# Optimization experiments

Hardware: AMD Instinct MI355X
Metric: run time of the kernel (lower is better)

Reference implementation:

```python
import jax, jax.numpy as jnp
import numpy as np

HEADS = 8
DIM_HEAD = 32
SCALE = DIM_HEAD ** (-0.5)


def setup_inputs() -> dict:
    key = jax.random.key(0)
    k1, k2, k3, k4 = jax.random.split(key, 4)
    x = jax.random.normal(k1, (16, 256, 64, 64), dtype=jnp.float32)
    # conv 1x1 weights stored as [out_ch, in_ch]
    w_qkv = jax.random.normal(k2, (3 * HEADS * DIM_HEAD, 256), dtype=jnp.float32) * 0.05
    w_out = jax.random.normal(k3, (256, HEADS * DIM_HEAD), dtype=jnp.float32) * 0.05
    b_out = jax.random.normal(k4, (256,), dtype=jnp.float32) * 0.05
    return {"x": x, "w_qkv": w_qkv, "w_out": w_out, "b_out": b_out}


def reference(x, w_qkv, w_out, b_out):
    b, c, h, w = x.shape
    n = h * w
    # 1x1 conv (no bias) == channel matmul
    qkv = jnp.einsum('bchw,oc->bohw', x, w_qkv)            # [b, 3*H*D, h, w]
    qkv = qkv.reshape(b, 3, HEADS, DIM_HEAD, n)            # chunk then 'b (h c) xy'
    q, k, v = qkv[:, 0], qkv[:, 1], qkv[:, 2]              # [b, H, D, n]
    q = jax.nn.softmax(q, axis=-2) * SCALE                 # softmax over channel dim d
    k = jax.nn.softmax(k, axis=-1)                         # softmax over spatial n
    context = jnp.einsum('bhdn,bhen->bhde', k, v)          # [b, H, D, D]
    out = jnp.einsum('bhde,bhdn->bhen', context, q)        # [b, H, D, n]
    out = out.reshape(b, HEADS * DIM_HEAD, h, w)
    # 1x1 conv with bias
    return jnp.einsum('bchw,oc->bohw', out, w_out) + b_out[None, :, None, None]
```

## Files before the change

kernel.cpp:

```cpp
#include <hip/hip_runtime.h>
#include <cstddef>
#include <cstdint>

#define NN 4096
#define CIN 256
#define CQKV 768
#define NBATCH 16
#define QSCALE 0.17677669529663687f

typedef short s16x8 __attribute__((ext_vector_type(8)));
typedef float f32x4 __attribute__((ext_vector_type(4)));

__device__ __forceinline__ float bf2f(unsigned short u) {
    unsigned int x = ((unsigned int)u) << 16;
    return __builtin_bit_cast(float, x);
}
__device__ __forceinline__ unsigned short f2bf(float f) {
    unsigned int u = __builtin_bit_cast(unsigned int, f);
    return (unsigned short)((u + 0x7fffu + ((u >> 16) & 1u)) >> 16);
}
__device__ __forceinline__ void glds16(const void* gsrc, void* lds) {
    __builtin_amdgcn_global_load_lds(
        (const __attribute__((address_space(1))) unsigned int*)gsrc,
        (__attribute__((address_space(3))) unsigned int*)lds,
        16, 0, 0);
}

__global__ __launch_bounds__(256)
void xpose(const float* __restrict__ x, unsigned short* __restrict__ xT)
{
    const int b = blockIdx.z;
    const int n0 = blockIdx.x * 64, c0 = blockIdx.y * 64;
    __shared__ float xs[64][65];
    const int t = threadIdx.x;
    const float* xb = x + (size_t)b * CIN * NN;
#pragma unroll
    for (int p = 0; p < 4; ++p) {
        const int row = p * 16 + (t >> 4);
        const int col = (t & 15) * 4;
        const float4 v = *reinterpret_cast<const float4*>(
            &xb[(size_t)(c0 + row) * NN + n0 + col]);
        xs[col + 0][row] = v.x; xs[col + 1][row] = v.y;
        xs[col + 2][row] = v.z; xs[col + 3][row] = v.w;
    }
    __syncthreads();
    const int n = t >> 2, cch = (t & 3) * 16;
    unsigned short arr[16];
#pragma unroll
    for (int e = 0; e < 16; ++e) arr[e] = f2bf(xs[n][cch + e]);
    unsigned short* dst = xT + ((size_t)b * NN + n0 + n) * 256 + c0 + cch;
    *reinterpret_cast<s16x8*>(&dst[0]) = *reinterpret_cast<s16x8*>(&arr[0]);
    *reinterpret_cast<s16x8*>(&dst[8]) = *reinterpret_cast<s16x8*>(&arr[8]);
}

__global__ __launch_bounds__(256)
void wcvt(const float* __restrict__ w, unsigned short* __restrict__ wb)
{
    const int i = (blockIdx.x * 256 + threadIdx.x) * 4;
    const float4 v = *reinterpret_cast<const float4*>(&w[i]);
    unsigned short a[4] = { f2bf(v.x), f2bf(v.y), f2bf(v.z), f2bf(v.w) };
    *reinterpret_cast<ushort2*>(&wb[i])     = *reinterpret_cast<ushort2*>(&a[0]);
    *reinterpret_cast<ushort2*>(&wb[i + 2]) = *reinterpret_cast<ushort2*>(&a[2]);
}

__device__ __forceinline__ void gemm_pipe(const unsigned short* __restrict__ Ab,
                                          const unsigned short* __restrict__ Bb,
                                          int m0, int n0, char* smem,
                                          f32x4 (&acc)[4][4])
{
    const int t = threadIdx.x;
    const int lane = t & 63, w = t >> 6;
    const int lr = lane & 15, lq = lane >> 4;
    const int wr = (w >> 1) * 64, wc = (w & 1) * 64;
    const int ch0 = (w * 2 + 0) * 64 + lane;
    const int ch1 = (w * 2 + 1) * 64 + lane;
    const int r0 = ch0 >> 2, c0s = (ch0 & 3) ^ ((r0 >> 1) & 3);
    const int r1 = ch1 >> 2, c1s = (ch1 & 3) ^ ((r1 >> 1) & 3);
    char* Abuf = smem;
    char* Bbuf = smem + 32768;

#define STG_H(h)                                                               \
  { char* ab = Abuf + ((h) & 3) * 8192;                                        \
    char* bb = Bbuf + ((h) & 3) * 8192;                                        \
    glds16(Ab + (size_t)(m0 + r0) * 256 + (h) * 32 + c0s * 8, ab + (w*2+0)*1024); \
    glds16(Ab + (size_t)(m0 + r1) * 256 + (h) * 32 + c1s * 8, ab + (w*2+1)*1024); \
    glds16(Bb + (size_t)(n0 + r0) * 256 + (h) * 32 + c0s * 8, bb + (w*2+0)*1024); \
    glds16(Bb + (size_t)(n0 + r1) * 256 + (h) * 32 + c1s * 8, bb + (w*2+1)*1024); }

#define CMP_H(h)                                                               \
  { char* ab = Abuf + ((h) & 3) * 8192;                                        \
    char* bb = Bbuf + ((h) & 3) * 8192;                                        \
    s16x8 af[4], bfr[4];                                                       \
    _Pragma("unroll") for (int m = 0; m < 4; ++m) {                            \
        const int row = wr + m * 16 + lr;                                      \
        af[m] = *(const s16x8*)(ab + row * 64 + ((lq ^ ((row >> 1) & 3)) << 4)); } \
    _Pragma("unroll") for (int n = 0; n < 4; ++n) {                            \
        const int col = wc + n * 16 + lr;                                      \
        bfr[n] = *(const s16x8*)(bb + col * 64 + ((lq ^ ((col >> 1) & 3)) << 4)); } \
    __builtin_amdgcn_s_setprio(1);                                             \
    _Pragma("unroll") for (int m = 0; m < 4; ++m)                              \
    _Pragma("unroll") for (int n = 0; n < 4; ++n)                              \
        acc[m][n] = __builtin_amdgcn_mfma_f32_16x16x32_bf16(af[m], bfr[n],     \
                                                            acc[m][n], 0, 0, 0); \
    __builtin_amdgcn_s_setprio(0); }

    STG_H(0); STG_H(1); STG_H(2);
#pragma unroll
    for (int i = 0; i < 8; ++i) {
        if (i < 6)       asm volatile("s_waitcnt vmcnt(8)" ::: "memory");
        else if (i == 6) asm volatile("s_waitcnt vmcnt(4)" ::: "memory");
        else             asm volatile("s_waitcnt vmcnt(0)" ::: "memory");
        __builtin_amdgcn_s_barrier();
        __builtin_amdgcn_sched_barrier(0);
        if (i < 5) STG_H(i + 3);
        CMP_H(i);
    }
#undef STG_H
#undef CMP_H
}

__global__ __launch_bounds__(256, 2)
void qkv_fused(const unsigned short* __restrict__ wb,
               const unsigned short* __restrict__ xT,
               unsigned short* __restrict__ qT,
               float* __restrict__ ctx_part,
               float* __restrict__ z_part)
{
    __shared__ __align__(16) char smem[65536];
    const int nt = blockIdx.x;
    const int ty = blockIdx.y;
    const int b  = blockIdx.z;
    const int t = threadIdx.x;
    const int lane = t & 63, w = t >> 6;
    const int lr = lane & 15, lq = lane >> 4;
    const int wr = (w >> 1) * 64, wc = (w & 1) * 64;
    const int n0 = nt * 128;

    if (ty < 2) {
        const int m0 = ty * 128;
        const unsigned short* Bb = xT + (size_t)b * NN * 256;
        f32x4 acc[4][4] = {};
        gemm_pipe(wb, Bb, m0, n0, smem, acc);

        __syncthreads();
        unsigned short (*qs)[136] = (unsigned short (*)[136])smem;
#pragma unroll
        for (int n = 0; n < 4; ++n) {
            const int col = wc + n * 16 + lr;
#pragma unroll
            for (int hp = 0; hp < 2; ++hp) {
                float mx = -1e30f;
#pragma unroll
                for (int u = 0; u < 2; ++u)
#pragma unroll
                    for (int r = 0; r < 4; ++r)
                        mx = fmaxf(mx, acc[hp * 2 + u][n][r]);
                mx = fmaxf(mx, __shfl_xor(mx, 16));
                mx = fmaxf(mx, __shfl_xor(mx, 32));
                float er[2][4];
                float s = 0.f;
#pragma unroll
                for (int u = 0; u < 2; ++u)
#pragma unroll
                    for (int r = 0; r < 4; ++r) {
                        er[u][r] = __expf(acc[hp * 2 + u][n][r] - mx);
                        s += er[u][r];
                    }
                s += __shfl_xor(s, 16);
                s += __shfl_xor(s, 32);
                const float inv = QSCALE / s;
#pragma unroll
                for (int u = 0; u < 2; ++u) {
                    ushort4 pk;
                    pk.x = f2bf(er[u][0] * inv);
                    pk.y = f2bf(er[u][1] * inv);
                    pk.z = f2bf(er[u][2] * inv);
                    pk.w = f2bf(er[u][3] * inv);
                    *(ushort4*)&qs[col][wr + (hp * 2 + u) * 16 + lq * 4] = pk;
                }
            }
        }
        __syncthreads();
        const int nl = t >> 1, half = t & 1;
        const unsigned short* src = &qs[nl][half * 64];
        unsigned short* dst = qT + ((size_t)b * NN + n0 + nl) * 256 + m0 + half * 64;
#pragma unroll
        for (int i = 0; i < 8; ++i)
            *(s16x8*)(dst + i * 8) = *(const s16x8*)(src + i * 8);
    } else {
        const int g = ty - 2;
        const unsigned short* An = xT + ((size_t)b * NN + (size_t)n0) * 256;

        f32x4 acc[4][4] = {};
        gemm_pipe(An, wb, 0, 256 + g * 128, smem, acc);

        unsigned int ekpk[4][4][2];
        float zl[4] = {0.f, 0.f, 0.f, 0.f};
#pragma unroll
        for (int m = 0; m < 4; ++m)
#pragma unroll
            for (int nn = 0; nn < 4; ++nn) {
                const unsigned short u0 = f2bf(__expf(acc[m][nn][0]));
                const unsigned short u1 = f2bf(__expf(acc[m][nn][1]));
                const unsigned short u2 = f2bf(__expf(acc[m][nn][2]));
                const unsigned short u3 = f2bf(__expf(acc[m][nn][3]));
                zl[nn] += bf2f(u0) + bf2f(u1) + bf2f(u2) + bf2f(u3);
                ekpk[m][nn][0] = (unsigned int)u0 | ((unsigned int)u1 << 16);
                ekpk[m][nn][1] = (unsigned int)u2 | ((unsigned int)u3 << 16);
            }
#pragma unroll
        for (int nn = 0; nn < 4; ++nn) {
            zl[nn] += __shfl_xor(zl[nn], 16);
            zl[nn] += __shfl_xor(zl[nn], 32);
        }
        const float zv = (lq == 0) ? zl[0] : (lq == 1) ? zl[1] : (lq == 2) ? zl[2] : zl[3];
        z_part[((((size_t)(b * 32 + nt)) * 2 + g) * 2 + (w >> 1)) * 128 + wc + lane] = zv;

#pragma unroll
        for (int m = 0; m < 4; ++m)
#pragma unroll
            for (int nn = 0; nn < 4; ++nn) acc[m][nn] = (f32x4){0.f, 0.f, 0.f, 0.f};
        gemm_pipe(An, wb, 0, 512 + g * 128, smem, acc);

        __syncthreads();
#pragma unroll
        for (int m = 0; m < 4; ++m)
#pragma unroll
            for (int nn = 0; nn < 4; ++nn) {
                const int col = wc + nn * 16 + lr;
                const int swz = (col & 7) << 4;
                const int rowb = (wr + m * 16 + lq * 4) * 2;
                *(unsigned int*)(smem + ((col * 256 + rowb) ^ swz))       = ekpk[m][nn][0];
                *(unsigned int*)(smem + ((col * 256 + rowb + 4) ^ swz))   = ekpk[m][nn][1];
                const unsigned int vp0 = (unsigned int)f2bf(acc[m][nn][0])
                                       | ((unsigned int)f2bf(acc[m][nn][1]) << 16);
                const unsigned int vp1 = (unsigned int)f2bf(acc[m][nn][2])
                                       | ((unsigned int)f2bf(acc[m][nn][3]) << 16);
                *(unsigned int*)(smem + 32768 + ((col * 256 + rowb) ^ swz))     = vp0;
                *(unsigned int*)(smem + 32768 + ((col * 256 + rowb + 4) ^ swz)) = vp1;
            }
        __syncthreads();

        f32x4 cacc[2][2] = {};
#pragma unroll
        for (int ks = 0; ks < 4; ++ks) {
            s16x8 af[2], bfv[2];
#pragma unroll
            for (int dt = 0; dt < 2; ++dt) {
                const int drow = w * 32 + dt * 16 + lr;
                af[dt] = *(const s16x8*)(smem +
                    ((drow * 256 + ks * 64 + lq * 16) ^ ((drow & 7) << 4)));
            }
#pragma unroll
            for (int et = 0; et < 2; ++et) {
                const int erow = w * 32 + et * 16 + lr;
                bfv[et] = *(const s16x8*)(smem + 32768 +
                    ((erow * 256 + ks * 64 + lq * 16) ^ ((erow & 7) << 4)));
            }
#pragma unroll
            for (int dt = 0; dt < 2; ++dt)
#pragma unroll
                for (int et = 0; et < 2; ++et)
                    cacc[dt][et] = __builtin_amdgcn_mfma_f32_16x16x32_bf16(
                        af[dt], bfv[et], cacc[dt][et], 0, 0, 0);
        }
        float* cp = ctx_part + ((((size_t)(b * 32 + nt)) * 2 + g) * 4 + w) * 1024;
#pragma unroll
        for (int dt = 0; dt < 2; ++dt)
#pragma unroll
            for (int et = 0; et < 2; ++et)
#pragma unroll
                for (int r = 0; r < 4; ++r)
                    cp[(dt * 16 + lq * 4 + r) * 32 + et * 16 + lr] = cacc[dt][et][r];
    }
}

__global__ __launch_bounds__(256)
void make_m(const float* __restrict__ ctx_part, const float* __restrict__ z_part,
            const float* __restrict__ w_out, unsigned short* __restrict__ Mmat)
{
    const int h = blockIdx.x, b = blockIdx.y;
    const int g = h >> 2, hh = h & 3;
    const int t = threadIdx.x;
    __shared__ float ctx[32][33];
    __shared__ float zinv[32];

    for (int c = t; c < 1024; c += 256) {
        float s = 0.f;
#pragma unroll 8
        for (int nt = 0; nt < 32; ++nt)
            s += ctx_part[((((size_t)(b * 32 + nt)) * 2 + g) * 4 + hh) * 1024 + c];
        ctx[c >> 5][c & 31] = s;
    }
    if (t < 32) {
        float z = 0.f;
#pragma unroll 8
        for (int nt = 0; nt < 32; ++nt) {
            const size_t base = (((size_t)(b * 32 + nt)) * 2 + g) * 2;
            z += z_part[(base + 0) * 128 + hh * 32 + t];
            z += z_part[(base + 1) * 128 + hh * 32 + t];
        }
        zinv[t] = 1.f / z;
    }
    __syncthreads();

    const int o = t;
    float wrow[32];
#pragma unroll
    for (int e = 0; e < 32; ++e)
        wrow[e] = w_out[(size_t)o * 256 + h * 32 + e];
#pragma unroll 4
    for (int d = 0; d < 32; ++d) {
        float s = 0.f;
#pragma unroll
        for (int e = 0; e < 32; ++e)
            s = fmaf(wrow[e], ctx[d][e], s);
        Mmat[((size_t)b * 256 + o) * 256 + h * 32 + d] = f2bf(s * zinv[d]);
    }
}

__global__ __launch_bounds__(256, 2)
void gemm_out(const unsigned short* __restrict__ Mmat,
              const unsigned short* __restrict__ qT,
              float* __restrict__ out, const float* __restrict__ bias)
{
    __shared__ __align__(16) char smem[65536];
    const int bz = blockIdx.z;
    const int m0 = blockIdx.y * 128, n0 = blockIdx.x * 128;
    const unsigned short* Ab = Mmat + (size_t)bz * 256 * 256;
    const unsigned short* Bb = qT + (size_t)bz * NN * 256;

    f32x4 acc[4][4] = {};
    gemm_pipe(Ab, Bb, m0, n0, smem, acc);

    const int t = threadIdx.x;
    const int lane = t & 63, w = t >> 6;
    const int lr = lane & 15, lq = lane >> 4;
    const int wr = (w >> 1) * 64, wc = (w & 1) * 64;

    __syncthreads();
#pragma unroll
    for (int m = 0; m < 4; ++m)
#pragma unroll
        for (int r = 0; r < 4; ++r) {
            const int row = wr + m * 16 + lq * 4 + r;
            const float bv = bias[m0 + row];
            const int rb = row * 512;
            const int xs = (row & 7) << 4;
#pragma unroll
            for (int n = 0; n < 4; ++n) {
                const int col = wc + n * 16 + lr;
                *(float*)(smem + rb + ((col * 4) ^ xs)) = acc[m][n][r] + bv;
            }
        }
    __syncthreads();

    float* Yb = out + (size_t)bz * CIN * NN;
#pragma unroll
    for (int p = 0; p < 8; ++p) {
        const int row = p * 16 + (t >> 4);
        const int rb = row * 512;
        const int xs = (row & 7) << 4;
        const int cb = (t & 15) * 32;
        const float4 v0 = *(const float4*)(smem + rb + ((cb + 0) ^ xs));
        const float4 v1 = *(const float4*)(smem + rb + ((cb + 16) ^ xs));
        float* dst = Yb + (size_t)(m0 + row) * NN + n0 + (t & 15) * 8;
        *(float4*)dst = v0;
        *(float4*)(dst + 4) = v1;
    }
}

extern "C" void kernel_launch(void* const* d_in, const int* in_sizes, int n_in,
                              void* d_out, int out_size, void* d_ws, size_t ws_size,
                              hipStream_t stream)
{
    const float* x     = (const float*)d_in[0];
    const float* w_qkv = (const float*)d_in[1];
    const float* w_out = (const float*)d_in[2];
    const float* b_out = (const float*)d_in[3];
    float* out = (float*)d_out;

    char* ws = (char*)d_ws;
    size_t off = 0;
    unsigned short* xT  = (unsigned short*)(ws + off);  off += (size_t)NBATCH * NN * CIN * 2;
    unsigned short* qT  = (unsigned short*)(ws + off);  off += (size_t)NBATCH * NN * CIN * 2;
    float* ctx_part     = (float*)(ws + off);           off += (size_t)NBATCH * 32 * 2 * 4 * 1024 * 4;
    float* z_part       = (float*)(ws + off);           off += (size_t)NBATCH * 32 * 2 * 2 * 128 * 4;
    unsigned short* Mmat= (unsigned short*)(ws + off);  off += (size_t)NBATCH * 256 * 256 * 2;
    unsigned short* wb  = (unsigned short*)(ws + off);  off += (size_t)CQKV * CIN * 2;

    xpose<<<dim3(NN / 64, CIN / 64, NBATCH), 256, 0, stream>>>(x, xT);
    wcvt<<<dim3(CQKV * CIN / 1024), 256, 0, stream>>>(w_qkv, wb);

    qkv_fused<<<dim3(32, 4, NBATCH), 256, 0, stream>>>(wb, xT, qT, ctx_part, z_part);

    make_m<<<dim3(8, NBATCH), 256, 0, stream>>>(ctx_part, z_part, w_out, Mmat);

    gemm_out<<<dim3(32, 2, NBATCH), 256, 0, stream>>>(Mmat, qT, out, b_out);
}
```

Before: 107.3 us.

## Shrink GEMM pipeline to three LDS stages to fit three blocks per CU

The shared GEMM pipeline drops from a 4-deep to a 3-deep LDS ring buffer, cutting shared memory from 64KB to 48KB per block. Launch bounds rise to 3 blocks per CU. The epilogues of qkv_fused (context MFMA staging) and gemm_out (output transpose) are split into two half passes so they fit in the smaller LDS. More resident blocks should hide latency better, at the cost of less prefetch depth, extra barriers in the epilogues, and register pressure under the tighter launch bound.

```diff
diff --git a/kernel.cpp b/kernel.cpp
--- a/kernel.cpp
+++ b/kernel.cpp
@@ -63,10 +63,10 @@
     *reinterpret_cast<ushort2*>(&wb[i + 2]) = *reinterpret_cast<ushort2*>(&a[2]);
 }
 
-__device__ __forceinline__ void gemm_pipe(const unsigned short* __restrict__ Ab,
-                                          const unsigned short* __restrict__ Bb,
-                                          int m0, int n0, char* smem,
-                                          f32x4 (&acc)[4][4])
+__device__ __forceinline__ void gemm_pipe3(const unsigned short* __restrict__ Ab,
+                                           const unsigned short* __restrict__ Bb,
+                                           int m0, int n0, char* smem,
+                                           f32x4 (&acc)[4][4])
 {
     const int t = threadIdx.x;
     const int lane = t & 63, w = t >> 6;
@@ -77,19 +77,19 @@
     const int r0 = ch0 >> 2, c0s = (ch0 & 3) ^ ((r0 >> 1) & 3);
     const int r1 = ch1 >> 2, c1s = (ch1 & 3) ^ ((r1 >> 1) & 3);
     char* Abuf = smem;
-    char* Bbuf = smem + 32768;
+    char* Bbuf = smem + 24576;
 
 #define STG_H(h)                                                               \
-  { char* ab = Abuf + ((h) & 3) * 8192;                                        \
-    char* bb = Bbuf + ((h) & 3) * 8192;                                        \
+  { char* ab = Abuf + ((h) % 3) * 8192;                                        \
+    char* bb = Bbuf + ((h) % 3) * 8192;                                        \
     glds16(Ab + (size_t)(m0 + r0) * 256 + (h) * 32 + c0s * 8, ab + (w*2+0)*1024); \
     glds16(Ab + (size_t)(m0 + r1) * 256 + (h) * 32 + c1s * 8, ab + (w*2+1)*1024); \
     glds16(Bb + (size_t)(n0 + r0) * 256 + (h) * 32 + c0s * 8, bb + (w*2+0)*1024); \
     glds16(Bb + (size_t)(n0 + r1) * 256 + (h) * 32 + c1s * 8, bb + (w*2+1)*1024); }
 
 #define CMP_H(h)                                                               \
-  { char* ab = Abuf + ((h) & 3) * 8192;                                        \
-    char* bb = Bbuf + ((h) & 3) * 8192;                                        \
+  { char* ab = Abuf + ((h) % 3) * 8192;                                        \
+    char* bb = Bbuf + ((h) % 3) * 8192;                                        \
     s16x8 af[4], bfr[4];                                                       \
     _Pragma("unroll") for (int m = 0; m < 4; ++m) {                            \
         const int row = wr + m * 16 + lr;                                      \
@@ -104,29 +104,28 @@
                                                             acc[m][n], 0, 0, 0); \
     __builtin_amdgcn_s_setprio(0); }
 
-    STG_H(0); STG_H(1); STG_H(2);
+    STG_H(0); STG_H(1);
 #pragma unroll
     for (int i = 0; i < 8; ++i) {
-        if (i < 6)       asm volatile("s_waitcnt vmcnt(8)" ::: "memory");
-        else if (i == 6) asm volatile("s_waitcnt vmcnt(4)" ::: "memory");
-        else             asm volatile("s_waitcnt vmcnt(0)" ::: "memory");
+        if (i < 7) asm volatile("s_waitcnt vmcnt(4)" ::: "memory");
+        else       asm volatile("s_waitcnt vmcnt(0)" ::: "memory");
         __builtin_amdgcn_s_barrier();
         __builtin_amdgcn_sched_barrier(0);
-        if (i < 5) STG_H(i + 3);
+        if (i < 6) STG_H(i + 2);
         CMP_H(i);
     }
 #undef STG_H
 #undef CMP_H
 }
 
-__global__ __launch_bounds__(256, 2)
+__global__ __launch_bounds__(256, 3)
 void qkv_fused(const unsigned short* __restrict__ wb,
                const unsigned short* __restrict__ xT,
                unsigned short* __restrict__ qT,
                float* __restrict__ ctx_part,
                float* __restrict__ z_part)
 {
-    __shared__ __align__(16) char smem[65536];
+    __shared__ __align__(16) char smem[49152];
     const int nt = blockIdx.x;
     const int ty = blockIdx.y;
     const int b  = blockIdx.z;
@@ -140,7 +139,7 @@
         const int m0 = ty * 128;
         const unsigned short* Bb = xT + (size_t)b * NN * 256;
         f32x4 acc[4][4] = {};
-        gemm_pipe(wb, Bb, m0, n0, smem, acc);
+        gemm_pipe3(wb, Bb, m0, n0, smem, acc);
 
         __syncthreads();
         unsigned short (*qs)[136] = (unsigned short (*)[136])smem;
@@ -192,7 +191,7 @@
         const unsigned short* An = xT + ((size_t)b * NN + (size_t)n0) * 256;
 
         f32x4 acc[4][4] = {};
-        gemm_pipe(An, wb, 0, 256 + g * 128, smem, acc);
+        gemm_pipe3(An, wb, 0, 256 + g * 128, smem, acc);
 
         unsigned int ekpk[4][4][2];
         float zl[4] = {0.f, 0.f, 0.f, 0.f};
@@ -220,49 +219,58 @@
         for (int m = 0; m < 4; ++m)
 #pragma unroll
             for (int nn = 0; nn < 4; ++nn) acc[m][nn] = (f32x4){0.f, 0.f, 0.f, 0.f};
-        gemm_pipe(An, wb, 0, 512 + g * 128, smem, acc);
+        gemm_pipe3(An, wb, 0, 512 + g * 128, smem, acc);
 
         __syncthreads();
-#pragma unroll
-        for (int m = 0; m < 4; ++m)
-#pragma unroll
-            for (int nn = 0; nn < 4; ++nn) {
-                const int col = wc + nn * 16 + lr;
-                const int swz = (col & 7) << 4;
-                const int rowb = (wr + m * 16 + lq * 4) * 2;
-                *(unsigned int*)(smem + ((col * 256 + rowb) ^ swz))       = ekpk[m][nn][0];
-                *(unsigned int*)(smem + ((col * 256 + rowb + 4) ^ swz))   = ekpk[m][nn][1];
-                const unsigned int vp0 = (unsigned int)f2bf(acc[m][nn][0])
-                                       | ((unsigned int)f2bf(acc[m][nn][1]) << 16);
-                const unsigned int vp1 = (unsigned int)f2bf(acc[m][nn][2])
-                                       | ((unsigned int)f2bf(acc[m][nn][3]) << 16);
-                *(unsigned int*)(smem + 32768 + ((col * 256 + rowb) ^ swz))     = vp0;
-                *(unsigned int*)(smem + 32768 + ((col * 256 + rowb + 4) ^ swz)) = vp1;
+        f32x4 cacc[2][2] = {};
+#pragma unroll
+        for (int p = 0; p < 2; ++p) {
+            if ((w >> 1) == p) {
+#pragma unroll
+                for (int m = 0; m < 4; ++m)
+#pragma unroll
+                    for (int nn = 0; nn < 4; ++nn) {
+                        const int col = wc + nn * 16 + lr;
+                        const int swz = (col & 7) << 4;
+                        const int rowb = (m * 16 + lq * 4) * 2;
+                        *(unsigned int*)(smem + ((col * 128 + rowb) ^ swz))
+                            = ekpk[m][nn][0];
+                        *(unsigned int*)(smem + ((col * 128 + rowb + 4) ^ swz))
+                            = ekpk[m][nn][1];
+                        const unsigned int vp0 = (unsigned int)f2bf(acc[m][nn][0])
+                            | ((unsigned int)f2bf(acc[m][nn][1]) << 16);
+                        const unsigned int vp1 = (unsigned int)f2bf(acc[m][nn][2])
+                            | ((unsigned int)f2bf(acc[m][nn][3]) << 16);
+                        *(unsigned int*)(smem + 16384 +
+                            ((col * 128 + rowb) ^ swz)) = vp0;
+                        *(unsigned int*)(smem + 16384 +
+                            ((col * 128 + rowb + 4) ^ swz)) = vp1;
+                    }
             }
-        __syncthreads();
-
-        f32x4 cacc[2][2] = {};
-#pragma unroll
-        for (int ks = 0; ks < 4; ++ks) {
-            s16x8 af[2], bfv[2];
-#pragma unroll
-            for (int dt = 0; dt < 2; ++dt) {
-                const int drow = w * 32 + dt * 16 + lr;
-                af[dt] = *(const s16x8*)(smem +
-                    ((drow * 256 + ks * 64 + lq * 16) ^ ((drow & 7) << 4)));
+            __syncthreads();
+#pragma unroll
+            for (int ks2 = 0; ks2 < 2; ++ks2) {
+                s16x8 afk[2], bfv[2];
+#pragma unroll
+                for (int dt = 0; dt < 2; ++dt) {
+                    const int drow = w * 32 + dt * 16 + lr;
+                    afk[dt] = *(const s16x8*)(smem + drow * 128 +
+                        ((((ks2 * 4 + lq) ^ (drow & 7))) << 4));
+                }
+#pragma unroll
+                for (int et = 0; et < 2; ++et) {
+                    const int erow = w * 32 + et * 16 + lr;
+                    bfv[et] = *(const s16x8*)(smem + 16384 + erow * 128 +
+                        ((((ks2 * 4 + lq) ^ (erow & 7))) << 4));
+                }
+#pragma unroll
+                for (int dt = 0; dt < 2; ++dt)
+#pragma unroll
+                    for (int et = 0; et < 2; ++et)
+                        cacc[dt][et] = __builtin_amdgcn_mfma_f32_16x16x32_bf16(
+                            afk[dt], bfv[et], cacc[dt][et], 0, 0, 0);
             }
-#pragma unroll
-            for (int et = 0; et < 2; ++et) {
-                const int erow = w * 32 + et * 16 + lr;
-                bfv[et] = *(const s16x8*)(smem + 32768 +
-                    ((erow * 256 + ks * 64 + lq * 16) ^ ((erow & 7) << 4)));
-            }
-#pragma unroll
-            for (int dt = 0; dt < 2; ++dt)
-#pragma unroll
-                for (int et = 0; et < 2; ++et)
-                    cacc[dt][et] = __builtin_amdgcn_mfma_f32_16x16x32_bf16(
-                        af[dt], bfv[et], cacc[dt][et], 0, 0, 0);
+            __syncthreads();
         }
         float* cp = ctx_part + ((((size_t)(b * 32 + nt)) * 2 + g) * 4 + w) * 1024;
 #pragma unroll
@@ -319,54 +327,59 @@
     }
 }
 
-__global__ __launch_bounds__(256, 2)
+__global__ __launch_bounds__(256, 3)
 void gemm_out(const unsigned short* __restrict__ Mmat,
               const unsigned short* __restrict__ qT,
               float* __restrict__ out, const float* __restrict__ bias)
 {
-    __shared__ __align__(16) char smem[65536];
+    __shared__ __align__(16) char smem[49152];
     const int bz = blockIdx.z;
     const int m0 = blockIdx.y * 128, n0 = blockIdx.x * 128;
     const unsigned short* Ab = Mmat + (size_t)bz * 256 * 256;
     const unsigned short* Bb = qT + (size_t)bz * NN * 256;
 
     f32x4 acc[4][4] = {};
-    gemm_pipe(Ab, Bb, m0, n0, smem, acc);
+    gemm_pipe3(Ab, Bb, m0, n0, smem, acc);
 
     const int t = threadIdx.x;
     const int lane = t & 63, w = t >> 6;
     const int lr = lane & 15, lq = lane >> 4;
-    const int wr = (w >> 1) * 64, wc = (w & 1) * 64;
+    const int wc = (w & 1) * 64;
 
     __syncthreads();
-#pragma unroll
-    for (int m = 0; m < 4; ++m)
-#pragma unroll
-        for (int r = 0; r < 4; ++r) {
-            const int row = wr + m * 16 + lq * 4 + r;
-            const float bv = bias[m0 + row];
-            const int rb = row * 512;
-            const int xs = (row & 7) << 4;
-#pragma unroll
-            for (int n = 0; n < 4; ++n) {
-                const int col = wc + n * 16 + lr;
-                *(float*)(smem + rb + ((col * 4) ^ xs)) = acc[m][n][r] + bv;
-            }
-        }
-    __syncthreads();
-
     float* Yb = out + (size_t)bz * CIN * NN;
 #pragma unroll
-    for (int p = 0; p < 8; ++p) {
-        const int row = p * 16 + (t >> 4);
-        const int rb = row * 512;
-        const int xs = (row & 7) << 4;
-        const int cb = (t & 15) * 32;
-        const float4 v0 = *(const float4*)(smem + rb + ((cb + 0) ^ xs));
-        const float4 v1 = *(const float4*)(smem + rb + ((cb + 16) ^ xs));
-        float* dst = Yb + (size_t)(m0 + row) * NN + n0 + (t & 15) * 8;
-        *(float4*)dst = v0;
-        *(float4*)(dst + 4) = v1;
+    for (int hf = 0; hf < 2; ++hf) {
+        if ((w >> 1) == hf) {
+#pragma unroll
+            for (int m = 0; m < 4; ++m)
+#pragma unroll
+                for (int r = 0; r < 4; ++r) {
+                    const int rl = m * 16 + lq * 4 + r;
+                    const float bv = bias[m0 + hf * 64 + rl];
+                    const int rb = rl * 512;
+                    const int xs = (rl & 7) << 4;
+#pragma unroll
+                    for (int n = 0; n < 4; ++n) {
+                        const int col = wc + n * 16 + lr;
+                        *(float*)(smem + rb + ((col * 4) ^ xs)) = acc[m][n][r] + bv;
+                    }
+                }
+        }
+        __syncthreads();
+#pragma unroll
+        for (int p = 0; p < 4; ++p) {
+            const int rl = p * 16 + (t >> 4);
+            const int rb = rl * 512;
+            const int xs = (rl & 7) << 4;
+            const int cb = (t & 15) * 32;
+            const float4 v0 = *(const float4*)(smem + rb + ((cb + 0) ^ xs));
+            const float4 v1 = *(const float4*)(smem + rb + ((cb + 16) ^ xs));
+            float* dst = Yb + (size_t)(m0 + hf * 64 + rl) * NN + n0 + (t & 15) * 8;
+            *(float4*)dst = v0;
+            *(float4*)(dst + 4) = v1;
+        }
+        __syncthreads();
     }
 }
 
```

Result: no change. 105.8 us (-1.4%).
